# Kernel tuning notes

Measured on AMD Instinct MI355X. Metric: run time of the kernel, lower is better.

The kernel has to match this reference:

```python
import jax, jax.numpy as jnp
import numpy as np

N = 8192
F_IN = 256
F_OUT = 128
SLOPE = 0.2
NEG_INF = -9000000000000000.0


def setup_inputs() -> dict:
    key = jax.random.key(0)
    k1, k2, k3, k4, k5 = jax.random.split(key, 5)
    x = jax.random.normal(k1, (N, F_IN), dtype=jnp.float32)
    adj = jax.random.randint(k2, (N, N), 0, 2).astype(jnp.float32)
    W = jax.random.normal(k3, (F_IN, F_OUT), dtype=jnp.float32) * (1.0 / np.sqrt(F_IN))
    a_src = jax.random.normal(k4, (F_OUT,), dtype=jnp.float32) * (1.0 / np.sqrt(F_OUT))
    a_dst = jax.random.normal(k5, (F_OUT,), dtype=jnp.float32) * (1.0 / np.sqrt(F_OUT))
    return {"x": x, "adj": adj, "W": W, "a_src": a_src, "a_dst": a_dst}


def reference(x, adj, W, a_src, a_dst):
    # h: (N, F_OUT)
    h = x @ W
    f_src = h @ a_src  # (N,)
    f_dst = h @ a_dst  # (N,)
    # additive attention scores: (N, N)
    e = f_src[:, None] + f_dst[None, :]
    e = jnp.where(e >= 0, e, SLOPE * e)  # leaky_relu
    e = jnp.where(adj > 0, e, NEG_INF)
    alpha = jax.nn.softmax(e, axis=1)  # (N, N)
    return alpha @ h  # (N, F_OUT)
```

## Files before the change

kernel.cpp:

```cpp
#include <hip/hip_runtime.h>
#include <hip/hip_bf16.h>

#define NN 8192
#define FIN 256
#define FO 128
#define JCHUNK 1024
#define NSTEP 16
#define L2E 1.4426950408889634f
#define C2  0.28853900817779268f

typedef __bf16 bf16x8 __attribute__((ext_vector_type(8)));
typedef __bf16 bf16x2 __attribute__((ext_vector_type(2)));
typedef float  f32x4  __attribute__((ext_vector_type(4)));
typedef unsigned long long u64;
typedef u64 u64x2 __attribute__((ext_vector_type(2)));

__global__ __launch_bounds__(256) void k_pack(
    const float* __restrict__ adj, u64* __restrict__ ab)
{
  const int tid = threadIdx.x;
  const int w = tid >> 6, lane = tid & 63;
  const int row = blockIdx.x * 4 + w;
  const float4* src = (const float4*)(adj + (size_t)row * NN) + lane;
  u64* dst = ab + (size_t)row * 128;

  for (int g = 0; g < 32; g += 2) {
    float4 va = src[g * 64];
    float4 vb = src[g * 64 + 64];
    u64 a0 = __ballot(va.x > 0.f);
    u64 a1 = __ballot(va.y > 0.f);
    u64 a2 = __ballot(va.z > 0.f);
    u64 a3 = __ballot(va.w > 0.f);
    if (lane < 4) {
      u64 m = lane == 0 ? a0 : lane == 1 ? a1 : lane == 2 ? a2 : a3;
      dst[g * 4 + lane] = m;
    }
    u64 b0 = __ballot(vb.x > 0.f);
    u64 b1 = __ballot(vb.y > 0.f);
    u64 b2 = __ballot(vb.z > 0.f);
    u64 b3 = __ballot(vb.w > 0.f);
    if (lane < 4) {
      u64 m = lane == 0 ? b0 : lane == 1 ? b1 : lane == 2 ? b2 : b3;
      dst[(g + 1) * 4 + lane] = m;
    }
  }
}

__global__ __launch_bounds__(256) void k_proj(
    const float* __restrict__ x, const float* __restrict__ W,
    const float* __restrict__ a_src, const float* __restrict__ a_dst,
    __bf16* __restrict__ Bp, float* __restrict__ f_src, float* __restrict__ f_dst)
{
  __shared__ float xs[16 * FIN];
  __shared__ float fs[16], fd[16];
  const int tid = threadIdx.x;
  const int i0 = blockIdx.x * 16;

  const float4* xg = (const float4*)(x + (size_t)i0 * FIN);
  float4* xs4 = (float4*)xs;
  #pragma unroll
  for (int t = 0; t < 4; t++) xs4[tid + 256 * t] = xg[tid + 256 * t];
  if (tid < 16) { fs[tid] = 0.f; fd[tid] = 0.f; }
  __syncthreads();

  const int cq = tid & 31;
  const int rg = tid >> 5;
  const int c0 = cq * 4;
  const int r0 = rg * 2;
  float acc0[4] = {0.f,0.f,0.f,0.f};
  float acc1[4] = {0.f,0.f,0.f,0.f};
  const float* xr0 = xs + r0 * FIN;
  const float* xr1 = xs + (r0 + 1) * FIN;

  for (int k = 0; k < FIN; k += 4) {
    float4 xa = *(const float4*)(xr0 + k);
    float4 xb = *(const float4*)(xr1 + k);
    #pragma unroll
    for (int kk = 0; kk < 4; kk++) {
      float4 wv = *(const float4*)(W + (size_t)(k + kk) * FO + c0);
      float xav = ((const float*)&xa)[kk];
      float xbv = ((const float*)&xb)[kk];
      acc0[0] += xav * wv.x; acc0[1] += xav * wv.y;
      acc0[2] += xav * wv.z; acc0[3] += xav * wv.w;
      acc1[0] += xbv * wv.x; acc1[1] += xbv * wv.y;
      acc1[2] += xbv * wv.z; acc1[3] += xbv * wv.w;
    }
  }

  float4 as = *(const float4*)(a_src + c0);
  float4 ad = *(const float4*)(a_dst + c0);
  float ps0 = acc0[0]*as.x + acc0[1]*as.y + acc0[2]*as.z + acc0[3]*as.w;
  float ps1 = acc1[0]*as.x + acc1[1]*as.y + acc1[2]*as.z + acc1[3]*as.w;
  float pd0 = acc0[0]*ad.x + acc0[1]*ad.y + acc0[2]*ad.z + acc0[3]*ad.w;
  float pd1 = acc1[0]*ad.x + acc1[1]*ad.y + acc1[2]*ad.z + acc1[3]*ad.w;
  atomicAdd(&fs[r0],     ps0);
  atomicAdd(&fs[r0 + 1], ps1);
  atomicAdd(&fd[r0],     pd0);
  atomicAdd(&fd[r0 + 1], pd1);

  const int j0 = i0 + r0;
  const int kg = j0 >> 5;
  const int q  = (j0 >> 3) & 3;
  const int t0 = j0 & 7;
  #pragma unroll
  for (int c = 0; c < 4; c++) {
    const int n = c0 + c;
    bf16x2 v;
    v[0] = (__bf16)acc0[c];
    v[1] = (__bf16)acc1[c];
    size_t idx = ((size_t)(kg * 8 + (n >> 4)) * 64 + q * 16 + (n & 15)) * 8 + t0;
    *(bf16x2*)(Bp + idx) = v;
  }
  __syncthreads();
  if (tid < 16) { f_src[i0 + tid] = fs[tid]; f_dst[i0 + tid] = fd[tid]; }
}

__global__ __launch_bounds__(256, 2) void k_attn(
    const u64* __restrict__ ab, const __bf16* __restrict__ Bp,
    const float* __restrict__ f_src, const float* __restrict__ f_dst,
    float* __restrict__ part, float* __restrict__ lpart)
{
  __shared__ float G1[JCHUNK];
  __shared__ float G2[JCHUNK];

  const int tid = threadIdx.x;
  const int rb = blockIdx.x >> 3;
  const int ks = blockIdx.x & 7;
  const int i0 = rb * 128;
  const int jbase = ks * JCHUNK;

  const int w = tid >> 6;
  const int lane = tid & 63;
  const int m = lane & 15;
  const int q = lane >> 4;
  const int wbase = i0 + w * 32;

  float F1[2], F2[2];
  #pragma unroll
  for (int mt = 0; mt < 2; mt++) {
    float s = f_src[wbase + mt * 16 + m];
    F1[mt] = __builtin_amdgcn_exp2f(s * L2E);
    F2[mt] = __builtin_amdgcn_exp2f(s * C2);
  }

  #pragma unroll
  for (int t = 0; t < 4; t++) {
    int j = tid + t * 256;
    float d = f_dst[jbase + j];
    G1[j] = __builtin_amdgcn_exp2f(d * L2E);
    G2[j] = __builtin_amdgcn_exp2f(d * C2);
  }
  __syncthreads();

  f32x4 acc[2][8];
  #pragma unroll
  for (int mt = 0; mt < 2; mt++)
    #pragma unroll
    for (int nt = 0; nt < 8; nt++) acc[mt][nt] = (f32x4){0.f, 0.f, 0.f, 0.f};
  float psum[2] = {0.f, 0.f};

  const u64* abm0 = ab + (size_t)(wbase + m) * 128 + ks * 16;
  const u64* abm1 = abm0 + (size_t)16 * 128;
  const __bf16* bsrc_base = Bp + (size_t)ks * 32 * 4096 + lane * 8;

  for (int sg = 0; sg < 4; ++sg) {
    u64x2 Ma01 = *(const u64x2*)(abm0 + sg * 4);
    u64x2 Ma23 = *(const u64x2*)(abm0 + sg * 4 + 2);
    u64x2 Mb01 = *(const u64x2*)(abm1 + sg * 4);
    u64x2 Mb23 = *(const u64x2*)(abm1 + sg * 4 + 2);

    #pragma unroll
    for (int ss = 0; ss < 4; ++ss) {
      const int step = sg * 4 + ss;
      #pragma unroll
      for (int kg = 0; kg < 2; kg++) {
        const int jj = step * 64 + kg * 32 + q * 8;
        float4 u0 = *(const float4*)(G1 + jj);
        float4 u1 = *(const float4*)(G1 + jj + 4);
        float4 v0 = *(const float4*)(G2 + jj);
        float4 v1 = *(const float4*)(G2 + jj + 4);
        const unsigned b = ss * 16 + kg * 8 + q * 2;

        bf16x8 af[2];
        #pragma unroll
        for (int mt = 0; mt < 2; mt++) {
          const u64 M0 = mt ? Mb01[0] : Ma01[0];
          const u64 M1 = mt ? Mb01[1] : Ma01[1];
          const u64 M2 = mt ? Mb23[0] : Ma23[0];
          const u64 M3 = mt ? Mb23[1] : Ma23[1];
          const unsigned e0 = (unsigned)(M0 >> b);
          const unsigned e1 = (unsigned)(M1 >> b);
          const unsigned e2 = (unsigned)(M2 >> b);
          const unsigned e3 = (unsigned)(M3 >> b);
          const float f1 = F1[mt], f2 = F2[mt];
          float p0 = (e0 & 1u) ? fmaxf(f1 * u0.x, f2 * v0.x) : 0.f;
          float p1 = (e1 & 1u) ? fmaxf(f1 * u0.y, f2 * v0.y) : 0.f;
          float p2 = (e2 & 1u) ? fmaxf(f1 * u0.z, f2 * v0.z) : 0.f;
          float p3 = (e3 & 1u) ? fmaxf(f1 * u0.w, f2 * v0.w) : 0.f;
          float p4 = (e0 & 2u) ? fmaxf(f1 * u1.x, f2 * v1.x) : 0.f;
          float p5 = (e1 & 2u) ? fmaxf(f1 * u1.y, f2 * v1.y) : 0.f;
          float p6 = (e2 & 2u) ? fmaxf(f1 * u1.z, f2 * v1.z) : 0.f;
          float p7 = (e3 & 2u) ? fmaxf(f1 * u1.w, f2 * v1.w) : 0.f;
          psum[mt] += ((p0 + p1) + (p2 + p3)) + ((p4 + p5) + (p6 + p7));
          bf16x8 a;
          a[0] = (__bf16)p0; a[1] = (__bf16)p1; a[2] = (__bf16)p2;
          a[3] = (__bf16)p3; a[4] = (__bf16)p4; a[5] = (__bf16)p5;
          a[6] = (__bf16)p6; a[7] = (__bf16)p7;
          af[mt] = a;
        }

        const __bf16* bsrc = bsrc_base + (size_t)(step * 2 + kg) * 4096;
        #pragma unroll
        for (int nt = 0; nt < 8; nt++) {
          bf16x8 bfrag = *(const bf16x8*)(bsrc + nt * 512);
          acc[0][nt] = __builtin_amdgcn_mfma_f32_16x16x32_bf16(af[0], bfrag, acc[0][nt], 0, 0, 0);
          acc[1][nt] = __builtin_amdgcn_mfma_f32_16x16x32_bf16(af[1], bfrag, acc[1][nt], 0, 0, 0);
        }
      }
    }
  }

  float* ldst = lpart + (size_t)ks * NN;
  #pragma unroll
  for (int mt = 0; mt < 2; mt++) {
    float p = psum[mt];
    p += __shfl_xor(p, 16);
    p += __shfl_xor(p, 32);
    if (lane < 16) ldst[wbase + mt * 16 + lane] = p;
  }

  float* pdst = part + (size_t)ks * NN * FO;
  #pragma unroll
  for (int mt = 0; mt < 2; mt++) {
    const int rb0 = wbase + mt * 16 + q * 4;
    #pragma unroll
    for (int nt = 0; nt < 8; nt++) {
      #pragma unroll
      for (int r = 0; r < 4; r++) {
        pdst[(size_t)(rb0 + r) * FO + nt * 16 + m] = acc[mt][nt][r];
      }
    }
  }
}

__global__ __launch_bounds__(256) void k_div(
    const float* __restrict__ part, const float* __restrict__ lpart,
    float* __restrict__ out)
{
  int idx = blockIdx.x * 256 + threadIdx.x;
  int row = idx >> 5;
  float4 s = {0.f, 0.f, 0.f, 0.f};
  float l = 0.f;
  #pragma unroll
  for (int ks = 0; ks < 8; ks++) {
    float4 v = ((const float4*)(part + (size_t)ks * NN * FO))[idx];
    s.x += v.x; s.y += v.y; s.z += v.z; s.w += v.w;
    l += lpart[ks * NN + row];
  }
  float inv = 1.0f / l;
  float4 o;
  o.x = s.x * inv; o.y = s.y * inv; o.z = s.z * inv; o.w = s.w * inv;
  ((float4*)out)[idx] = o;
}

extern "C" void kernel_launch(void* const* d_in, const int* in_sizes, int n_in,
                              void* d_out, int out_size, void* d_ws, size_t ws_size,
                              hipStream_t stream) {
  const float* x     = (const float*)d_in[0];
  const float* adj   = (const float*)d_in[1];
  const float* W     = (const float*)d_in[2];
  const float* a_src = (const float*)d_in[3];
  const float* a_dst = (const float*)d_in[4];
  float* out = (float*)d_out;

  char* ws = (char*)d_ws;
  __bf16* Bp   = (__bf16*)ws;
  float* f_src = (float*)(ws + 2097152);
  float* f_dst = (float*)(ws + 2097152 + 32768);
  u64*   ab    = (u64*)(ws + 4194304);
  float* part  = (float*)(ws + 16777216);
  float* lpart = (float*)(ws + 50331648);

  hipLaunchKernelGGL(k_pack, dim3(2048), dim3(256), 0, stream, adj, ab);
  hipLaunchKernelGGL(k_proj, dim3(512), dim3(256), 0, stream,
                     x, W, a_src, a_dst, Bp, f_src, f_dst);
  hipLaunchKernelGGL(k_attn, dim3(512), dim3(256), 0, stream,
                     ab, Bp, f_src, f_dst, part, lpart);
  hipLaunchKernelGGL(k_div, dim3(1024), dim3(256), 0, stream,
                     part, lpart, out);
}
```

Before: 471.7 us.

## Fuse adjacency bitmask packing into attention kernel and double the K split

Removes the separate k_pack kernel. Each attention block now reads its own 128x512 tile of the fp32 adjacency matrix, ballots it into bitmasks and keeps them in shared memory. The column split grows from 8 to 16 so the grid has 1024 blocks, and the occupancy hint of 2 in the launch bounds is dropped. This saves one launch and the round trip of the packed mask through global memory. In exchange the partial-output buffer doubles in size, k_div has twice as much reduction traffic, and the mask loads now sit on the attention kernel's critical path.

New measurement: 468.2 us. No clear change (-0.7%).

```diff
diff --git a/kernel.cpp b/kernel.cpp
--- a/kernel.cpp
+++ b/kernel.cpp
@@ -4,8 +4,11 @@
 #define NN 8192
 #define FIN 256
 #define FO 128
-#define JCHUNK 1024
-#define NSTEP 16
+#define KSPLIT 16
+#define JCHUNK 512
+#define NSTEP 8
+#define SGN 2
+#define MSTRIDE 10
 #define L2E 1.4426950408889634f
 #define C2  0.28853900817779268f
 
@@ -14,37 +17,6 @@
 typedef float  f32x4  __attribute__((ext_vector_type(4)));
 typedef unsigned long long u64;
 typedef u64 u64x2 __attribute__((ext_vector_type(2)));
-
-__global__ __launch_bounds__(256) void k_pack(
-    const float* __restrict__ adj, u64* __restrict__ ab)
-{
-  const int tid = threadIdx.x;
-  const int w = tid >> 6, lane = tid & 63;
-  const int row = blockIdx.x * 4 + w;
-  const float4* src = (const float4*)(adj + (size_t)row * NN) + lane;
-  u64* dst = ab + (size_t)row * 128;
-
-  for (int g = 0; g < 32; g += 2) {
-    float4 va = src[g * 64];
-    float4 vb = src[g * 64 + 64];
-    u64 a0 = __ballot(va.x > 0.f);
-    u64 a1 = __ballot(va.y > 0.f);
-    u64 a2 = __ballot(va.z > 0.f);
-    u64 a3 = __ballot(va.w > 0.f);
-    if (lane < 4) {
-      u64 m = lane == 0 ? a0 : lane == 1 ? a1 : lane == 2 ? a2 : a3;
-      dst[g * 4 + lane] = m;
-    }
-    u64 b0 = __ballot(vb.x > 0.f);
-    u64 b1 = __ballot(vb.y > 0.f);
-    u64 b2 = __ballot(vb.z > 0.f);
-    u64 b3 = __ballot(vb.w > 0.f);
-    if (lane < 4) {
-      u64 m = lane == 0 ? b0 : lane == 1 ? b1 : lane == 2 ? b2 : b3;
-      dst[(g + 1) * 4 + lane] = m;
-    }
-  }
-}
 
 __global__ __launch_bounds__(256) void k_proj(
     const float* __restrict__ x, const float* __restrict__ W,
@@ -115,17 +87,18 @@
   if (tid < 16) { f_src[i0 + tid] = fs[tid]; f_dst[i0 + tid] = fd[tid]; }
 }
 
-__global__ __launch_bounds__(256, 2) void k_attn(
-    const u64* __restrict__ ab, const __bf16* __restrict__ Bp,
+__global__ __launch_bounds__(256) void k_attn(
+    const float* __restrict__ adj, const __bf16* __restrict__ Bp,
     const float* __restrict__ f_src, const float* __restrict__ f_dst,
     float* __restrict__ part, float* __restrict__ lpart)
 {
   __shared__ float G1[JCHUNK];
   __shared__ float G2[JCHUNK];
+  __shared__ __align__(16) u64 msk[128][MSTRIDE];
 
   const int tid = threadIdx.x;
-  const int rb = blockIdx.x >> 3;
-  const int ks = blockIdx.x & 7;
+  const int rb = blockIdx.x >> 4;
+  const int ks = blockIdx.x & 15;
   const int i0 = rb * 128;
   const int jbase = ks * JCHUNK;
 
@@ -144,7 +117,7 @@
   }
 
   #pragma unroll
-  for (int t = 0; t < 4; t++) {
+  for (int t = 0; t < 2; t++) {
     int j = tid + t * 256;
     float d = f_dst[jbase + j];
     G1[j] = __builtin_amdgcn_exp2f(d * L2E);
@@ -152,6 +125,28 @@
   }
   __syncthreads();
 
+  const float* abase = adj + (size_t)wbase * NN + jbase + lane * 4;
+  #pragma unroll 2
+  for (int rr = 0; rr < 32; ++rr) {
+    const float* rp = abase + (size_t)rr * NN;
+    float4 c0 = *(const float4*)rp;
+    float4 c1 = *(const float4*)(rp + 256);
+    u64 w00 = __ballot(c0.x > 0.f);
+    u64 w01 = __ballot(c0.y > 0.f);
+    u64 w02 = __ballot(c0.z > 0.f);
+    u64 w03 = __ballot(c0.w > 0.f);
+    u64 w10 = __ballot(c1.x > 0.f);
+    u64 w11 = __ballot(c1.y > 0.f);
+    u64 w12 = __ballot(c1.z > 0.f);
+    u64 w13 = __ballot(c1.w > 0.f);
+    if (lane < 8) {
+      u64 v = lane == 0 ? w00 : lane == 1 ? w01 : lane == 2 ? w02 :
+              lane == 3 ? w03 : lane == 4 ? w10 : lane == 5 ? w11 :
+              lane == 6 ? w12 : w13;
+      msk[w * 32 + rr][lane] = v;
+    }
+  }
+
   f32x4 acc[2][8];
   #pragma unroll
   for (int mt = 0; mt < 2; mt++)
@@ -159,15 +154,14 @@
     for (int nt = 0; nt < 8; nt++) acc[mt][nt] = (f32x4){0.f, 0.f, 0.f, 0.f};
   float psum[2] = {0.f, 0.f};
 
-  const u64* abm0 = ab + (size_t)(wbase + m) * 128 + ks * 16;
-  const u64* abm1 = abm0 + (size_t)16 * 128;
-  const __bf16* bsrc_base = Bp + (size_t)ks * 32 * 4096 + lane * 8;
-
-  for (int sg = 0; sg < 4; ++sg) {
-    u64x2 Ma01 = *(const u64x2*)(abm0 + sg * 4);
-    u64x2 Ma23 = *(const u64x2*)(abm0 + sg * 4 + 2);
-    u64x2 Mb01 = *(const u64x2*)(abm1 + sg * 4);
-    u64x2 Mb23 = *(const u64x2*)(abm1 + sg * 4 + 2);
+  const int r0l = w * 32 + m;
+  const __bf16* bsrc_base = Bp + (size_t)ks * 16 * 4096 + lane * 8;
+
+  for (int sg = 0; sg < SGN; ++sg) {
+    u64x2 Ma01 = *(const u64x2*)&msk[r0l][sg * 4];
+    u64x2 Ma23 = *(const u64x2*)&msk[r0l][sg * 4 + 2];
+    u64x2 Mb01 = *(const u64x2*)&msk[r0l + 16][sg * 4];
+    u64x2 Mb23 = *(const u64x2*)&msk[r0l + 16][sg * 4 + 2];
 
     #pragma unroll
     for (int ss = 0; ss < 4; ++ss) {
@@ -252,7 +246,7 @@
   float4 s = {0.f, 0.f, 0.f, 0.f};
   float l = 0.f;
   #pragma unroll
-  for (int ks = 0; ks < 8; ks++) {
+  for (int ks = 0; ks < KSPLIT; ks++) {
     float4 v = ((const float4*)(part + (size_t)ks * NN * FO))[idx];
     s.x += v.x; s.y += v.y; s.z += v.z; s.w += v.w;
     l += lpart[ks * NN + row];
@@ -277,15 +271,13 @@
   __bf16* Bp   = (__bf16*)ws;
   float* f_src = (float*)(ws + 2097152);
   float* f_dst = (float*)(ws + 2097152 + 32768);
-  u64*   ab    = (u64*)(ws + 4194304);
   float* part  = (float*)(ws + 16777216);
-  float* lpart = (float*)(ws + 50331648);
-
-  hipLaunchKernelGGL(k_pack, dim3(2048), dim3(256), 0, stream, adj, ab);
+  float* lpart = (float*)(ws + 83886080);
+
   hipLaunchKernelGGL(k_proj, dim3(512), dim3(256), 0, stream,
                      x, W, a_src, a_dst, Bp, f_src, f_dst);
-  hipLaunchKernelGGL(k_attn, dim3(512), dim3(256), 0, stream,
-                     ab, Bp, f_src, f_dst, part, lpart);
+  hipLaunchKernelGGL(k_attn, dim3(1024), dim3(256), 0, stream,
+                     adj, Bp, f_src, f_dst, part, lpart);
   hipLaunchKernelGGL(k_div, dim3(1024), dim3(256), 0, stream,
                      part, lpart, out);
 }
```
